# Kernel optimization log

Measured on AMD Instinct MI355X. Metric: run time of the kernel, lower is better.

The kernel has to match this reference:

```python
import jax, jax.numpy as jnp
import numpy as np

TINY = 1e-6
MIN_DEG, MAX_DEG = 0, 16

# 3x21 icosahedral basis used for the background (non-diag) IPE
P = jnp.asarray(np.array([
    0.8506508, 0.0, 0.5257311, 0.809017, 0.5, 0.309017, 0.5257311, 0.8506508, 0.0,
    1.0, 0.0, 0.0, 0.809017, 0.5, -0.309017, 0.8506508, 0.0, -0.5257311, 0.309017,
    0.809017, -0.5, 0.0, 0.5257311, -0.8506508, 0.5, 0.309017, -0.809017, 0.0, 1.0,
    0.0, -0.5257311, 0.8506508, 0.0, -0.309017, 0.809017, -0.5, 0.0, 0.5257311,
    0.8506508, -0.309017, 0.809017, 0.5, 0.309017, 0.809017, 0.5, 0.5, 0.309017,
    0.809017, 0.5, -0.309017, 0.809017, 0.0, 0.0, 1.0, -0.5, 0.309017, 0.809017,
    -0.809017, 0.5, 0.309017, -0.809017, 0.5, -0.309017], dtype=np.float32).reshape(3, 21))


def setup_inputs() -> dict:
    key = jax.random.key(0)
    k1, k2, k3, k4, k5 = jax.random.split(key, 5)
    N, Ns = 2048, 64
    ray_o = jax.random.normal(k1, (N, 3), dtype=jnp.float32)
    ray_d = jax.random.normal(k2, (N, 3), dtype=jnp.float32)
    fg_z_vals = jnp.sort(jax.random.uniform(k3, (N, Ns + 1), minval=0.1, maxval=5.0), axis=-1)
    bg_z_vals = jnp.sort(jax.random.uniform(k4, (N, Ns + 1), minval=1.0, maxval=50.0), axis=-1)
    radii = jax.random.uniform(k5, (N, 1), minval=0.005, maxval=0.02)
    return {"ray_o": ray_o, "ray_d": ray_d, "fg_z_vals": fg_z_vals,
            "bg_z_vals": bg_z_vals, "radii": radii}


def _frustum_moments(t0, t1, base_radius):
    mu = (t0 + t1) / 2.0
    hw = (t1 - t0) / 2.0
    denom = 3.0 * mu ** 2 + hw ** 2
    t_mean = mu + 2.0 * mu * hw ** 2 / denom
    t_var = hw ** 2 / 3.0 - (4.0 / 15.0) * (hw ** 4 * (12.0 * mu ** 2 - hw ** 2) / denom ** 2)
    r_var = base_radius ** 2 * (mu ** 2 / 4.0 + (5.0 / 12.0) * hw ** 2 - (4.0 / 15.0) * hw ** 4 / denom)
    return t_mean, t_var, r_var


def cast_rays_diag(t_vals, origins, directions, radii):
    t_mean, t_var, r_var = _frustum_moments(t_vals[..., :-1], t_vals[..., 1:], radii)
    d = directions[..., None, :]                      # [N,1,3]
    mean = d * t_mean[..., None]                      # [N,Ns,3]
    d_mag_sq = jnp.maximum(1e-8, jnp.sum(d ** 2, axis=-1, keepdims=True))
    d_outer_diag = d ** 2
    null_outer_diag = 1.0 - d_outer_diag / d_mag_sq
    cov_diag = t_var[..., None] * d_outer_diag + r_var[..., None] * null_outer_diag
    return mean + origins[..., None, :], cov_diag


def cast_rays_full(t_vals, origins, directions, radii):
    t_mean, t_var, r_var = _frustum_moments(t_vals[..., :-1], t_vals[..., 1:], radii)
    d = directions[..., None, :]                      # [N,1,3]
    mean = d * t_mean[..., None]                      # [N,Ns,3]
    d_mag_sq = jnp.maximum(1e-8, jnp.sum(d ** 2, axis=-1, keepdims=True))
    d_outer = d[..., :, None] * d[..., None, :]       # [N,1,3,3]
    eye = jnp.eye(3, dtype=d.dtype)
    null_outer = eye - d[..., :, None] * (d / d_mag_sq)[..., None, :]
    cov = t_var[..., None, None] * d_outer + r_var[..., None, None] * null_outer
    return mean + origins[..., None, :], cov          # [N,Ns,3], [N,Ns,3,3]


def _contract_point(x):
    n = jnp.linalg.norm(x) + TINY
    return (2.0 - 1.0 / n) * (x / n)


def contract_gaussian(mean, cov_full):
    N, Ns = mean.shape[0], mean.shape[1]
    flat = mean.reshape(-1, 3)
    J = jax.vmap(jax.jacfwd(_contract_point))(flat).reshape(N, Ns, 3, 3)
    n = jnp.linalg.norm(mean, axis=-1, keepdims=True) + TINY
    mean_c = (2.0 - 1.0 / n) * (mean / n)
    cov_c = jnp.einsum('nsij,nsjk,nslk->nsil', J, cov_full, J)
    return mean_c, cov_c


def expected_sin(x, x_var):
    return jnp.exp(-0.5 * x_var) * jnp.sin(x)


def ipe_diag(x, x_cov_diag, min_deg, max_deg):
    scales = 2.0 ** jnp.arange(min_deg, max_deg, dtype=x.dtype)   # [L]
    N, Ns = x.shape[0], x.shape[1]
    y = (x[..., None, :] * scales[:, None]).reshape(N, Ns, -1)                 # [N,Ns,L*3]
    y_var = (x_cov_diag[..., None, :] * (scales ** 2)[:, None]).reshape(N, Ns, -1)
    return expected_sin(jnp.concatenate([y, y + 0.5 * jnp.pi], axis=-1),
                        jnp.concatenate([y_var, y_var], axis=-1))


def ipe_full(x, x_cov, min_deg, max_deg):
    y = jnp.matmul(x, P)                                                        # [N,Ns,21]
    y_var = jnp.einsum('nsab,bk,ak->nsk', x_cov, P, P)                          # [N,Ns,21]
    scales = 2.0 ** jnp.arange(min_deg, max_deg, dtype=x.dtype)
    N, Ns = x.shape[0], x.shape[1]
    y = (y[..., None, :] * scales[:, None]).reshape(N, Ns, -1)                  # [N,Ns,L*21]
    y_var = (y_var[..., None, :] * (scales ** 2)[:, None]).reshape(N, Ns, -1)
    return expected_sin(jnp.concatenate([y, y + 0.5 * jnp.pi], axis=-1),
                        jnp.concatenate([y_var, y_var], axis=-1))


def reference(ray_o, ray_d, fg_z_vals, bg_z_vals, radii):
    # foreground: diagonal-cov cone cast + diagonal IPE  -> [N,Ns,96]
    fg_mean, fg_cov_diag = cast_rays_diag(fg_z_vals, ray_o, ray_d, radii)
    enc_fg = ipe_diag(fg_mean, fg_cov_diag, MIN_DEG, MAX_DEG)
    # background: full-cov cone cast + contraction Jacobian + basis IPE -> [N,Ns,672]
    bg_mean, bg_cov = cast_rays_full(bg_z_vals, ray_o, ray_d, radii)
    mean_c, cov_c = contract_gaussian(bg_mean, bg_cov)
    enc_bg = ipe_full(mean_c, cov_c, MIN_DEG, MAX_DEG)
    return jnp.concatenate([enc_fg, enc_bg], axis=-1)                            # [N,Ns,768]
```

## Files before the change

kernel.cpp:

```cpp
#include <hip/hip_runtime.h>
#include <math.h>

#define NS 64
#define INV2PI  0.15915494309189535f
#define NEGHL2E (-0.72134752044448170f)

typedef __attribute__((ext_vector_type(4))) float vfloat4;

__constant__ float c_P[63] = {
  0.8506508f, 0.0f, 0.5257311f, 0.809017f, 0.5f, 0.309017f, 0.5257311f,
  0.8506508f, 0.0f, 1.0f, 0.0f, 0.0f, 0.809017f, 0.5f, -0.309017f,
  0.8506508f, 0.0f, -0.5257311f, 0.309017f, 0.809017f, -0.5f,
  0.0f, 0.5257311f, -0.8506508f, 0.5f, 0.309017f, -0.809017f, 0.0f, 1.0f,
  0.0f, -0.5257311f, 0.8506508f, 0.0f, -0.309017f, 0.809017f, -0.5f, 0.0f,
  0.5257311f, 0.8506508f, -0.309017f, 0.809017f, 0.5f,
  0.309017f, 0.809017f, 0.5f, 0.5f, 0.309017f, 0.809017f, 0.5f, -0.309017f,
  0.809017f, 0.0f, 0.0f, 1.0f, -0.5f, 0.309017f, 0.809017f, -0.809017f,
  0.5f, 0.309017f, -0.809017f, 0.5f, -0.309017f
};

struct DescTab768 { unsigned v[768]; };
static constexpr DescTab768 make_desc768() {
    DescTab768 t{};
    for (int c = 0; c < 768; ++c) {
        int deg, src, ph;
        if      (c < 48)  { deg = c / 3;               src = 21 + c % 3;        ph = 0; }
        else if (c < 96)  { int cc = c - 48;  deg = cc / 3;  src = 21 + cc % 3; ph = 1; }
        else if (c < 432) { int cc = c - 96;  deg = cc / 21; src = cc % 21;     ph = 0; }
        else              { int cc = c - 432; deg = cc / 21; src = cc % 21;     ph = 1; }
        t.v[c] = ((unsigned)(127 + deg) << 23) | ((unsigned)src << 3) | (unsigned)ph;
    }
    return t;
}
__constant__ DescTab768 cDesc = make_desc768();

struct Moments { float t_mean, t_var, r_var; };

__device__ inline Moments frustum_moments(float t0, float t1, float radius) {
    float mu  = 0.5f * (t0 + t1);
    float hw  = 0.5f * (t1 - t0);
    float mu2 = mu * mu, hw2 = hw * hw;
    float denom = 3.0f * mu2 + hw2;
    float inv_d = 1.0f / denom;
    float hw4 = hw2 * hw2;
    Moments m;
    m.t_mean = mu + 2.0f * mu * hw2 * inv_d;
    m.t_var  = hw2 * (1.0f / 3.0f)
             - (4.0f / 15.0f) * (hw4 * (12.0f * mu2 - hw2) * inv_d * inv_d);
    m.r_var  = radius * radius *
               (0.25f * mu2 + (5.0f / 12.0f) * hw2 - (4.0f / 15.0f) * hw4 * inv_d);
    return m;
}

__device__ inline void emit4(uint4 d, const char* __restrict__ rowXV, float* __restrict__ o) {
    vfloat4 v;
    {
        unsigned wd = d.x;
        float sf = __uint_as_float(wd & 0xFF800000u);
        float2 xv = *reinterpret_cast<const float2*>(rowXV + (wd & 0xF8u));
        float e  = __builtin_amdgcn_exp2f(xv.y * (sf * sf));
        float ph = (float)(wd & 1u) * 0.25f;
        v.x = e * __builtin_amdgcn_sinf(__builtin_amdgcn_fractf(xv.x * sf + ph));
    }
    {
        unsigned wd = d.y;
        float sf = __uint_as_float(wd & 0xFF800000u);
        float2 xv = *reinterpret_cast<const float2*>(rowXV + (wd & 0xF8u));
        float e  = __builtin_amdgcn_exp2f(xv.y * (sf * sf));
        float ph = (float)(wd & 1u) * 0.25f;
        v.y = e * __builtin_amdgcn_sinf(__builtin_amdgcn_fractf(xv.x * sf + ph));
    }
    {
        unsigned wd = d.z;
        float sf = __uint_as_float(wd & 0xFF800000u);
        float2 xv = *reinterpret_cast<const float2*>(rowXV + (wd & 0xF8u));
        float e  = __builtin_amdgcn_exp2f(xv.y * (sf * sf));
        float ph = (float)(wd & 1u) * 0.25f;
        v.z = e * __builtin_amdgcn_sinf(__builtin_amdgcn_fractf(xv.x * sf + ph));
    }
    {
        unsigned wd = d.w;
        float sf = __uint_as_float(wd & 0xFF800000u);
        float2 xv = *reinterpret_cast<const float2*>(rowXV + (wd & 0xF8u));
        float e  = __builtin_amdgcn_exp2f(xv.y * (sf * sf));
        float ph = (float)(wd & 1u) * 0.25f;
        v.w = e * __builtin_amdgcn_sinf(__builtin_amdgcn_fractf(xv.x * sf + ph));
    }
    __builtin_nontemporal_store(v, reinterpret_cast<vfloat4*>(o));
}

__global__ __launch_bounds__(256, 4) void mipnerf_enc(
    const float* __restrict__ ray_o,
    const float* __restrict__ ray_d,
    const float* __restrict__ fgz,
    const float* __restrict__ bgz,
    const float* __restrict__ radii,
    float* __restrict__ out)
{
    const int n   = blockIdx.x;
    const int tid = threadIdx.x;

    __shared__ float sXV[NS * 50];
    __shared__ float sCore[NS * 11];
    __shared__ __align__(16) unsigned sD[768];

    const float ox = ray_o[3 * n + 0], oy = ray_o[3 * n + 1], oz = ray_o[3 * n + 2];
    const float dx = ray_d[3 * n + 0], dy = ray_d[3 * n + 1], dz = ray_d[3 * n + 2];
    const float rad = radii[n];
    const float dm = fmaxf(1e-8f, dx * dx + dy * dy + dz * dz);
    const float inv_dm = 1.0f / dm;

    if (tid < NS) {
        const int s = tid;
        {
            float t0 = fgz[(NS + 1) * n + s];
            float t1 = fgz[(NS + 1) * n + s + 1];
            Moments mm = frustum_moments(t0, t1, rad);
            float d3[3] = {dx, dy, dz};
            float o3[3] = {ox, oy, oz};
            #pragma unroll
            for (int i = 0; i < 3; ++i) {
                float m  = o3[i] + d3[i] * mm.t_mean;
                float dd = d3[i] * d3[i];
                float cd = mm.t_var * dd + mm.r_var * (1.0f - dd * inv_dm);
                sXV[s * 50 + 2 * (21 + i) + 0] = m  * INV2PI;
                sXV[s * 50 + 2 * (21 + i) + 1] = cd * NEGHL2E;
            }
        }
        {
            float t0 = bgz[(NS + 1) * n + s];
            float t1 = bgz[(NS + 1) * n + s + 1];
            Moments mm = frustum_moments(t0, t1, rad);
            float x0 = ox + dx * mm.t_mean;
            float x1 = oy + dy * mm.t_mean;
            float x2 = oz + dz * mm.t_mean;
            float a  = mm.t_var - mm.r_var * inv_dm;
            float rv = mm.r_var;
            float rn2 = x0 * x0 + x1 * x1 + x2 * x2;
            float rn  = sqrtf(rn2);
            float nn  = rn + 1e-6f;
            float inn = 1.0f / nn;
            float g   = (2.0f * nn - 1.0f) * inn * inn;
            float gp  = 2.0f * (1.0f - nn) * inn * inn * inn;
            float h   = gp / rn;
            float xd  = x0 * dx + x1 * dy + x2 * dz;
            float hxd = h * xd;
            float u0 = g * dx + hxd * x0;
            float u1 = g * dy + hxd * x1;
            float u2 = g * dz + hxd * x2;
            float w  = 2.0f * g * h + h * h * rn2;
            float* cr = &sCore[s * 11];
            cr[0] = x0; cr[1] = x1; cr[2] = x2;
            cr[3] = u0; cr[4] = u1; cr[5] = u2;
            cr[6] = g;  cr[7] = a;  cr[8] = rv * g * g; cr[9] = rv * w;
        }
    } else {
        for (int e = tid - NS; e < 768; e += 256 - NS) sD[e] = cDesc.v[e];
    }
    __syncthreads();

    #pragma unroll
    for (int j = 0; j < 6; ++j) {
        int i = tid + 256 * j;
        if (i < 21 * NS) {
            int k = i >> 6;
            int s = i & (NS - 1);
            const float p0 = c_P[k], p1 = c_P[21 + k], p2 = c_P[42 + k];
            const float* cr = &sCore[s * 11];
            float x0 = cr[0], x1 = cr[1], x2 = cr[2];
            float u0 = cr[3], u1 = cr[4], u2 = cr[5];
            float g = cr[6], c1 = cr[7], c2 = cr[8], c3 = cr[9];
            float dpx = p0 * x0 + p1 * x1 + p2 * x2;
            float dpu = p0 * u0 + p1 * u1 + p2 * u2;
            float pp  = p0 * p0 + p1 * p1 + p2 * p2;
            float y   = g * dpx;
            float yv  = c1 * dpu * dpu + c2 * pp + c3 * dpx * dpx;
            sXV[s * 50 + 2 * k + 0] = y  * INV2PI;
            sXV[s * 50 + 2 * k + 1] = yv * NEGHL2E;
        }
    }
    __syncthreads();

    const int lane = tid & 63;
    const int w    = tid >> 6;
    const uint4* sD4 = reinterpret_cast<const uint4*>(sD);
    const uint4 d0 = sD4[lane];
    const uint4 d1 = sD4[64 + lane];
    const uint4 d2 = sD4[128 + lane];

    float* __restrict__ outp = out + (size_t)n * (NS * 768);

    for (int ss = 0; ss < 16; ++ss) {
        const int s = w * 16 + ss;
        const char* rowXV = reinterpret_cast<const char*>(&sXV[s * 50]);
        float* orow = outp + s * 768 + lane * 4;
        emit4(d0, rowXV, orow);
        emit4(d1, rowXV, orow + 256);
        emit4(d2, rowXV, orow + 512);
    }
}

extern "C" void kernel_launch(void* const* d_in, const int* in_sizes, int n_in,
                              void* d_out, int out_size, void* d_ws, size_t ws_size,
                              hipStream_t stream) {
    const float* ray_o = (const float*)d_in[0];
    const float* ray_d = (const float*)d_in[1];
    const float* fgz   = (const float*)d_in[2];
    const float* bgz   = (const float*)d_in[3];
    const float* radii = (const float*)d_in[4];
    float* out = (float*)d_out;
    const int N = in_sizes[0] / 3;
    mipnerf_enc<<<N, 256, 0, stream>>>(ray_o, ray_d, fgz, bgz, radii, out);
}
```

Measured before the change: 406.7 us.

## Make sample precompute wave-local and drop block barriers and descriptor LDS copy

Each wave now computes the projected means and variances for its own 16 samples, with 4 lanes per sample splitting the 21+3 basis columns. Because a wave only reads rows it wrote itself, both __syncthreads and the sCore staging buffer are dropped and replaced by an LDS wait. The descriptor table is read straight from constant memory instead of being copied into shared memory first. The cost is that the frustum moments and contraction Jacobian are computed redundantly by all 4 lanes of each sample group.

```diff
diff --git a/kernel.cpp b/kernel.cpp
--- a/kernel.cpp
+++ b/kernel.cpp
@@ -97,12 +97,14 @@
     const float* __restrict__ radii,
     float* __restrict__ out)
 {
-    const int n   = blockIdx.x;
-    const int tid = threadIdx.x;
+    const int n    = blockIdx.x;
+    const int tid  = threadIdx.x;
+    const int lane = tid & 63;
+    const int wid  = tid >> 6;
+    const int sub  = lane & 3;
+    const int s    = wid * 16 + (lane >> 2);
 
     __shared__ float sXV[NS * 50];
-    __shared__ float sCore[NS * 11];
-    __shared__ __align__(16) unsigned sD[768];
 
     const float ox = ray_o[3 * n + 0], oy = ray_o[3 * n + 1], oz = ray_o[3 * n + 2];
     const float dx = ray_d[3 * n + 0], dy = ray_d[3 * n + 1], dz = ray_d[3 * n + 2];
@@ -110,90 +112,72 @@
     const float dm = fmaxf(1e-8f, dx * dx + dy * dy + dz * dz);
     const float inv_dm = 1.0f / dm;
 
-    if (tid < NS) {
-        const int s = tid;
-        {
-            float t0 = fgz[(NS + 1) * n + s];
-            float t1 = fgz[(NS + 1) * n + s + 1];
-            Moments mm = frustum_moments(t0, t1, rad);
-            float d3[3] = {dx, dy, dz};
-            float o3[3] = {ox, oy, oz};
-            #pragma unroll
-            for (int i = 0; i < 3; ++i) {
-                float m  = o3[i] + d3[i] * mm.t_mean;
-                float dd = d3[i] * d3[i];
-                float cd = mm.t_var * dd + mm.r_var * (1.0f - dd * inv_dm);
-                sXV[s * 50 + 2 * (21 + i) + 0] = m  * INV2PI;
-                sXV[s * 50 + 2 * (21 + i) + 1] = cd * NEGHL2E;
+    {
+        float t0 = fgz[(NS + 1) * n + s];
+        float t1 = fgz[(NS + 1) * n + s + 1];
+        Moments mm = frustum_moments(t0, t1, rad);
+        if (sub < 3) {
+            float d3 = (sub == 0) ? dx : ((sub == 1) ? dy : dz);
+            float o3 = (sub == 0) ? ox : ((sub == 1) ? oy : oz);
+            float m  = o3 + d3 * mm.t_mean;
+            float dd = d3 * d3;
+            float cd = mm.t_var * dd + mm.r_var * (1.0f - dd * inv_dm);
+            sXV[s * 50 + 2 * (21 + sub) + 0] = m  * INV2PI;
+            sXV[s * 50 + 2 * (21 + sub) + 1] = cd * NEGHL2E;
+        }
+    }
+    {
+        float t0 = bgz[(NS + 1) * n + s];
+        float t1 = bgz[(NS + 1) * n + s + 1];
+        Moments mm = frustum_moments(t0, t1, rad);
+        float x0 = ox + dx * mm.t_mean;
+        float x1 = oy + dy * mm.t_mean;
+        float x2 = oz + dz * mm.t_mean;
+        float a  = mm.t_var - mm.r_var * inv_dm;
+        float rv = mm.r_var;
+        float rn2 = x0 * x0 + x1 * x1 + x2 * x2;
+        float rn  = sqrtf(rn2);
+        float nn  = rn + 1e-6f;
+        float inn = 1.0f / nn;
+        float g   = (2.0f * nn - 1.0f) * inn * inn;
+        float gp  = 2.0f * (1.0f - nn) * inn * inn * inn;
+        float h   = gp / rn;
+        float xd  = x0 * dx + x1 * dy + x2 * dz;
+        float hxd = h * xd;
+        float u0 = g * dx + hxd * x0;
+        float u1 = g * dy + hxd * x1;
+        float u2 = g * dz + hxd * x2;
+        float jw = 2.0f * g * h + h * h * rn2;
+        float c1 = a, c2 = rv * g * g, c3 = rv * jw;
+        #pragma unroll
+        for (int j = 0; j < 6; ++j) {
+            int k = sub + 4 * j;
+            if (k < 21) {
+                const float p0 = c_P[k], p1 = c_P[21 + k], p2 = c_P[42 + k];
+                float dpx = p0 * x0 + p1 * x1 + p2 * x2;
+                float dpu = p0 * u0 + p1 * u1 + p2 * u2;
+                float pp  = p0 * p0 + p1 * p1 + p2 * p2;
+                float y   = g * dpx;
+                float yv  = c1 * dpu * dpu + c2 * pp + c3 * dpx * dpx;
+                sXV[s * 50 + 2 * k + 0] = y  * INV2PI;
+                sXV[s * 50 + 2 * k + 1] = yv * NEGHL2E;
             }
         }
-        {
-            float t0 = bgz[(NS + 1) * n + s];
-            float t1 = bgz[(NS + 1) * n + s + 1];
-            Moments mm = frustum_moments(t0, t1, rad);
-            float x0 = ox + dx * mm.t_mean;
-            float x1 = oy + dy * mm.t_mean;
-            float x2 = oz + dz * mm.t_mean;
-            float a  = mm.t_var - mm.r_var * inv_dm;
-            float rv = mm.r_var;
-            float rn2 = x0 * x0 + x1 * x1 + x2 * x2;
-            float rn  = sqrtf(rn2);
-            float nn  = rn + 1e-6f;
-            float inn = 1.0f / nn;
-            float g   = (2.0f * nn - 1.0f) * inn * inn;
-            float gp  = 2.0f * (1.0f - nn) * inn * inn * inn;
-            float h   = gp / rn;
-            float xd  = x0 * dx + x1 * dy + x2 * dz;
-            float hxd = h * xd;
-            float u0 = g * dx + hxd * x0;
-            float u1 = g * dy + hxd * x1;
-            float u2 = g * dz + hxd * x2;
-            float w  = 2.0f * g * h + h * h * rn2;
-            float* cr = &sCore[s * 11];
-            cr[0] = x0; cr[1] = x1; cr[2] = x2;
-            cr[3] = u0; cr[4] = u1; cr[5] = u2;
-            cr[6] = g;  cr[7] = a;  cr[8] = rv * g * g; cr[9] = rv * w;
-        }
-    } else {
-        for (int e = tid - NS; e < 768; e += 256 - NS) sD[e] = cDesc.v[e];
     }
-    __syncthreads();
 
-    #pragma unroll
-    for (int j = 0; j < 6; ++j) {
-        int i = tid + 256 * j;
-        if (i < 21 * NS) {
-            int k = i >> 6;
-            int s = i & (NS - 1);
-            const float p0 = c_P[k], p1 = c_P[21 + k], p2 = c_P[42 + k];
-            const float* cr = &sCore[s * 11];
-            float x0 = cr[0], x1 = cr[1], x2 = cr[2];
-            float u0 = cr[3], u1 = cr[4], u2 = cr[5];
-            float g = cr[6], c1 = cr[7], c2 = cr[8], c3 = cr[9];
-            float dpx = p0 * x0 + p1 * x1 + p2 * x2;
-            float dpu = p0 * u0 + p1 * u1 + p2 * u2;
-            float pp  = p0 * p0 + p1 * p1 + p2 * p2;
-            float y   = g * dpx;
-            float yv  = c1 * dpu * dpu + c2 * pp + c3 * dpx * dpx;
-            sXV[s * 50 + 2 * k + 0] = y  * INV2PI;
-            sXV[s * 50 + 2 * k + 1] = yv * NEGHL2E;
-        }
-    }
-    __syncthreads();
+    asm volatile("s_waitcnt lgkmcnt(0)" ::: "memory");
 
-    const int lane = tid & 63;
-    const int w    = tid >> 6;
-    const uint4* sD4 = reinterpret_cast<const uint4*>(sD);
-    const uint4 d0 = sD4[lane];
-    const uint4 d1 = sD4[64 + lane];
-    const uint4 d2 = sD4[128 + lane];
+    const uint4* cD4 = reinterpret_cast<const uint4*>(cDesc.v);
+    const uint4 d0 = cD4[lane];
+    const uint4 d1 = cD4[64 + lane];
+    const uint4 d2 = cD4[128 + lane];
 
     float* __restrict__ outp = out + (size_t)n * (NS * 768);
 
     for (int ss = 0; ss < 16; ++ss) {
-        const int s = w * 16 + ss;
-        const char* rowXV = reinterpret_cast<const char*>(&sXV[s * 50]);
-        float* orow = outp + s * 768 + lane * 4;
+        const int se = wid * 16 + ss;
+        const char* rowXV = reinterpret_cast<const char*>(&sXV[se * 50]);
+        float* orow = outp + se * 768 + lane * 4;
         emit4(d0, rowXV, orow);
         emit4(d1, rowXV, orow + 256);
         emit4(d2, rowXV, orow + 512);
```

Measured after the change: 408.7 us. Within noise of the previous version (+0.5%).
